# Optimization experiments

Measured on AMD Instinct MI355X. Metric: run time of the kernel, lower is better.

## Reference

```python
import jax, jax.numpy as jnp
import numpy as np

B, F, E = 2048, 200, 64

def setup_inputs() -> dict:
    key = jax.random.key(0)
    k1, k2 = jax.random.split(key)
    feature = jax.random.normal(k1, (B, F, E), dtype=jnp.float32)
    # nn.init.normal(weight, mean=0, std=0.01)
    weight = 0.01 * jax.random.normal(k2, (F, E, E), dtype=jnp.float32)
    return {"feature": feature, "weight": weight}

def reference(feature, weight):
    # biLinear[b,i,d] = sum_e feature[b,i,e] * weight[i,e,d]   (per-feature bilinear projection)
    bilinear = jnp.einsum('bie,ied->bid', feature, weight)
    # out[b,i,j] = sum_d bilinear[b,i,d] * feature[b,j,d]      (pairwise dot, avoids (B,F,F,E) temp)
    out = jnp.einsum('bid,bjd->bij', bilinear, feature)
    return out
```

## Files before the change

kernel.cpp:

```cpp
#include <hip/hip_runtime.h>

constexpr int Bb = 2048, Ff = 200, Ee = 64;

__global__ __launch_bounds__(256, 4)
void k1_bilinear(const float* __restrict__ feat, const float* __restrict__ wgt,
                 float* __restrict__ bil) {
    __shared__ float At[Ee * 64];
    __shared__ float Wl[Ee * 64];
    const int i  = blockIdx.y;
    const int b0 = blockIdx.x << 6;
    const int t  = threadIdx.x;

    {
        const float4* src = reinterpret_cast<const float4*>(wgt + (size_t)i * Ee * Ee);
        float4* dst = reinterpret_cast<float4*>(Wl);
        for (int q = t; q < 1024; q += 256) dst[q] = src[q];
    }
    for (int q = t; q < 1024; q += 256) {
        const int r  = q >> 4;
        const int e0 = (q & 15) << 2;
        const float4 v = *reinterpret_cast<const float4*>(
            feat + ((size_t)(b0 + r) * Ff + i) * Ee + e0);
        const int rf4 = r >> 2, rm = r & 3;
        const float vv[4] = {v.x, v.y, v.z, v.w};
#pragma unroll
        for (int k = 0; k < 4; ++k) {
            const int e = e0 + k;
            At[e * 64 + (((rf4 ^ ((e >> 2) & 7)) << 2) | rm)] = vv[k];
        }
    }
    __syncthreads();

    const int tx = t & 15, ty = t >> 4;
    const int d0 = tx << 2;
    float acc[4][4] = {};
#pragma unroll 4
    for (int e = 0; e < Ee; ++e) {
        const float4 a = *reinterpret_cast<const float4*>(
            At + e * 64 + ((ty ^ ((e >> 2) & 7)) << 2));
        const float4 w = *reinterpret_cast<const float4*>(Wl + e * 64 + d0);
        const float av[4] = {a.x, a.y, a.z, a.w};
        const float wv[4] = {w.x, w.y, w.z, w.w};
#pragma unroll
        for (int r = 0; r < 4; ++r)
#pragma unroll
            for (int c = 0; c < 4; ++c)
                acc[r][c] = fmaf(av[r], wv[c], acc[r][c]);
    }
#pragma unroll
    for (int r = 0; r < 4; ++r) {
        const float4 v = {acc[r][0], acc[r][1], acc[r][2], acc[r][3]};
        *reinterpret_cast<float4*>(
            bil + ((size_t)(b0 + (ty << 2) + r) * Ff + i) * Ee + d0) = v;
    }
}

__global__ __launch_bounds__(256, 2)
void k2_outer(const float* __restrict__ feat, const float* __restrict__ bil,
              float* __restrict__ out) {
    __shared__ float fT[Ee * 224];
    __shared__ float bT[Ee * 64];
    const int b = blockIdx.x;
    const int t = threadIdx.x;

    for (int q = t; q < 3200; q += 256) {
        const int j  = q >> 4;
        const int d0 = (q & 15) << 2;
        const float4 v = *reinterpret_cast<const float4*>(
            feat + ((size_t)b * Ff + j) * Ee + d0);
        const int jf4 = j >> 2, jm = j & 3;
        const float vv[4] = {v.x, v.y, v.z, v.w};
#pragma unroll
        for (int k = 0; k < 4; ++k) {
            const int d = d0 + k;
            fT[d * 224 + (((jf4 ^ ((d >> 2) & 7)) << 2) | jm)] = vv[k];
        }
    }

    const int jt = t % 50;
    const int it = t / 50;

    for (int i0 = 0; i0 < Ff; i0 += 40) {
        for (int q = t; q < 640; q += 256) {
            const int r  = q >> 4;
            const int d0 = (q & 15) << 2;
            const float4 v = *reinterpret_cast<const float4*>(
                bil + ((size_t)b * Ff + i0 + r) * Ee + d0);
            const int rf4 = r >> 2, rm = r & 3;
            const float vv[4] = {v.x, v.y, v.z, v.w};
#pragma unroll
            for (int k = 0; k < 4; ++k) {
                const int d = d0 + k;
                bT[d * 64 + (((rf4 ^ ((d >> 2) & 7)) << 2) | rm)] = vv[k];
            }
        }
        __syncthreads();

        if (t < 250) {
            float acc[8][4] = {};
#pragma unroll 4
            for (int d = 0; d < Ee; ++d) {
                const int c = (d >> 2) & 7;
                const float4 w4 = *reinterpret_cast<const float4*>(
                    fT + d * 224 + ((jt ^ c) << 2));
                const float4 a0 = *reinterpret_cast<const float4*>(
                    bT + d * 64 + (((it * 2) ^ c) << 2));
                const float4 a1 = *reinterpret_cast<const float4*>(
                    bT + d * 64 + (((it * 2 + 1) ^ c) << 2));
                const float av[8] = {a0.x, a0.y, a0.z, a0.w, a1.x, a1.y, a1.z, a1.w};
                const float wv[4] = {w4.x, w4.y, w4.z, w4.w};
#pragma unroll
                for (int r = 0; r < 8; ++r)
#pragma unroll
                    for (int c2 = 0; c2 < 4; ++c2)
                        acc[r][c2] = fmaf(av[r], wv[c2], acc[r][c2]);
            }
#pragma unroll
            for (int r = 0; r < 8; ++r) {
                const int i = i0 + it * 8 + r;
                const float4 v = {acc[r][0], acc[r][1], acc[r][2], acc[r][3]};
                *reinterpret_cast<float4*>(
                    out + ((size_t)b * Ff + i) * Ff + (jt << 2)) = v;
            }
        }
        __syncthreads();
    }
}

extern "C" void kernel_launch(void* const* d_in, const int* in_sizes, int n_in,
                              void* d_out, int out_size, void* d_ws, size_t ws_size,
                              hipStream_t stream) {
    const float* feat = (const float*)d_in[0];
    const float* wgt  = (const float*)d_in[1];
    float* out = (float*)d_out;
    float* bil = (float*)d_ws;

    k1_bilinear<<<dim3(Bb / 64, Ff), 256, 0, stream>>>(feat, wgt, bil);
    k2_outer<<<Bb, 256, 0, stream>>>(feat, bil, out);
}
```

Measured before the change: 558.8 us.

## Use split-bf16 MFMA for both bilinear and pairwise GEMMs

Both kernels are rewritten to run on bf16 MFMA instructions. Each fp32 operand is split into a high and a low bf16 half, and three MFMAs per tile approximate fp32 precision. The intermediate bilinear tensor is stored as packed hi/lo bf16 pairs. The second kernel now splits each batch across two blocks of 512 threads with per-wave 16-row strips. This trades scalar FMA work for matrix-core throughput, with roughly 3x the MFMA count and some loss of precision from dropping the lo*lo term. Output stores become scalar and strided per lane instead of float4.

```diff
diff --git a/kernel.cpp b/kernel.cpp
--- a/kernel.cpp
+++ b/kernel.cpp
@@ -1,129 +1,193 @@
 #include <hip/hip_runtime.h>
 
+
+typedef short bx8  __attribute__((ext_vector_type(8)));
+typedef float f32x4 __attribute__((ext_vector_type(4)));
+
 constexpr int Bb = 2048, Ff = 200, Ee = 64;
 
-__global__ __launch_bounds__(256, 4)
+__device__ __forceinline__ ushort bf16h(float x) {
+    uint u = __float_as_uint(x);
+    return (ushort)((u + 0x7FFFu + ((u >> 16) & 1u)) >> 16);
+}
+__device__ __forceinline__ float bf16f(ushort h) {
+    return __uint_as_float(((uint)h) << 16);
+}
+
+__global__ __launch_bounds__(256, 3)
 void k1_bilinear(const float* __restrict__ feat, const float* __restrict__ wgt,
-                 float* __restrict__ bil) {
-    __shared__ float At[Ee * 64];
-    __shared__ float Wl[Ee * 64];
+                 uint* __restrict__ bilP) {
+    __shared__ ushort fH[128 * 64], fL[128 * 64];
+    __shared__ ushort wH[64 * 64],  wL[64 * 64];
     const int i  = blockIdx.y;
-    const int b0 = blockIdx.x << 6;
+    const int b0 = blockIdx.x << 7;
     const int t  = threadIdx.x;
 
-    {
-        const float4* src = reinterpret_cast<const float4*>(wgt + (size_t)i * Ee * Ee);
-        float4* dst = reinterpret_cast<float4*>(Wl);
-        for (int q = t; q < 1024; q += 256) dst[q] = src[q];
-    }
-    for (int q = t; q < 1024; q += 256) {
-        const int r  = q >> 4;
-        const int e0 = (q & 15) << 2;
+    for (int q = t; q < 2048; q += 256) {
+        const int row = q >> 4, e0 = (q & 15) << 2;
         const float4 v = *reinterpret_cast<const float4*>(
-            feat + ((size_t)(b0 + r) * Ff + i) * Ee + e0);
-        const int rf4 = r >> 2, rm = r & 3;
+            feat + ((size_t)(b0 + row) * Ff + i) * Ee + e0);
         const float vv[4] = {v.x, v.y, v.z, v.w};
-#pragma unroll
-        for (int k = 0; k < 4; ++k) {
-            const int e = e0 + k;
-            At[e * 64 + (((rf4 ^ ((e >> 2) & 7)) << 2) | rm)] = vv[k];
-        }
+        ushort hh[4], ll[4];
+#pragma unroll
+        for (int j = 0; j < 4; ++j) {
+            hh[j] = bf16h(vv[j]);
+            ll[j] = bf16h(vv[j] - bf16f(hh[j]));
+        }
+        const int idx = row * 64 + (e0 ^ ((row & 7) << 3));
+        *reinterpret_cast<ushort4*>(&fH[idx]) = make_ushort4(hh[0], hh[1], hh[2], hh[3]);
+        *reinterpret_cast<ushort4*>(&fL[idx]) = make_ushort4(ll[0], ll[1], ll[2], ll[3]);
+    }
+    for (int q = t; q < 2048; q += 256) {
+        const int e = (q >> 6) << 1;
+        const int d = q & 63;
+        const float x0 = wgt[((size_t)i * Ee + e) * Ee + d];
+        const float x1 = wgt[((size_t)i * Ee + e + 1) * Ee + d];
+        const ushort h0 = bf16h(x0), h1 = bf16h(x1);
+        const ushort l0 = bf16h(x0 - bf16f(h0)), l1 = bf16h(x1 - bf16f(h1));
+        const int idx = d * 64 + (e ^ ((d & 7) << 3));
+        *reinterpret_cast<uint*>(&wH[idx]) = (uint)h0 | ((uint)h1 << 16);
+        *reinterpret_cast<uint*>(&wL[idx]) = (uint)l0 | ((uint)l1 << 16);
     }
     __syncthreads();
 
-    const int tx = t & 15, ty = t >> 4;
-    const int d0 = tx << 2;
-    float acc[4][4] = {};
-#pragma unroll 4
-    for (int e = 0; e < Ee; ++e) {
-        const float4 a = *reinterpret_cast<const float4*>(
-            At + e * 64 + ((ty ^ ((e >> 2) & 7)) << 2));
-        const float4 w = *reinterpret_cast<const float4*>(Wl + e * 64 + d0);
-        const float av[4] = {a.x, a.y, a.z, a.w};
-        const float wv[4] = {w.x, w.y, w.z, w.w};
-#pragma unroll
-        for (int r = 0; r < 4; ++r)
-#pragma unroll
-            for (int c = 0; c < 4; ++c)
-                acc[r][c] = fmaf(av[r], wv[c], acc[r][c]);
-    }
-#pragma unroll
-    for (int r = 0; r < 4; ++r) {
-        const float4 v = {acc[r][0], acc[r][1], acc[r][2], acc[r][3]};
-        *reinterpret_cast<float4*>(
-            bil + ((size_t)(b0 + (ty << 2) + r) * Ff + i) * Ee + d0) = v;
-    }
-}
-
-__global__ __launch_bounds__(256, 2)
-void k2_outer(const float* __restrict__ feat, const float* __restrict__ bil,
+    const int lane = t & 63, w = t >> 6;
+    const int r16 = lane & 15, g = lane >> 4;
+    f32x4 acc[2][4];
+#pragma unroll
+    for (int a = 0; a < 2; ++a)
+#pragma unroll
+        for (int j = 0; j < 4; ++j) acc[a][j] = (f32x4){0.f, 0.f, 0.f, 0.f};
+
+#pragma unroll
+    for (int ks = 0; ks < 2; ++ks) {
+        const int coff = ks * 32 + (g << 3);
+        bx8 AH[2], AL[2];
+#pragma unroll
+        for (int it = 0; it < 2; ++it) {
+            const int row = (w * 2 + it) * 16 + r16;
+            const int idx = row * 64 + (coff ^ ((row & 7) << 3));
+            AH[it] = *reinterpret_cast<const bx8*>(&fH[idx]);
+            AL[it] = *reinterpret_cast<const bx8*>(&fL[idx]);
+        }
+#pragma unroll
+        for (int jt = 0; jt < 4; ++jt) {
+            const int col = jt * 16 + r16;
+            const int idx = col * 64 + (coff ^ ((col & 7) << 3));
+            const bx8 BH = *reinterpret_cast<const bx8*>(&wH[idx]);
+            const bx8 BL = *reinterpret_cast<const bx8*>(&wL[idx]);
+#pragma unroll
+            for (int it = 0; it < 2; ++it) {
+                acc[it][jt] = __builtin_amdgcn_mfma_f32_16x16x32_bf16(AH[it], BH, acc[it][jt], 0, 0, 0);
+                acc[it][jt] = __builtin_amdgcn_mfma_f32_16x16x32_bf16(AH[it], BL, acc[it][jt], 0, 0, 0);
+                acc[it][jt] = __builtin_amdgcn_mfma_f32_16x16x32_bf16(AL[it], BH, acc[it][jt], 0, 0, 0);
+            }
+        }
+    }
+#pragma unroll
+    for (int it = 0; it < 2; ++it) {
+#pragma unroll
+        for (int jt = 0; jt < 4; ++jt) {
+            const int d = jt * 16 + r16;
+#pragma unroll
+            for (int reg = 0; reg < 4; ++reg) {
+                const int brow = b0 + (w * 2 + it) * 16 + (g << 2) + reg;
+                const float x = acc[it][jt][reg];
+                const ushort h = bf16h(x);
+                const ushort l = bf16h(x - bf16f(h));
+                bilP[((size_t)brow * Ff + i) * Ee + d] = (uint)h | ((uint)l << 16);
+            }
+        }
+    }
+}
+
+__global__ __launch_bounds__(512, 4)
+void k2_outer(const float* __restrict__ feat, const uint* __restrict__ bilP,
               float* __restrict__ out) {
-    __shared__ float fT[Ee * 224];
-    __shared__ float bT[Ee * 64];
-    const int b = blockIdx.x;
+    __shared__ ushort fjH[208 * 32], fjL[208 * 32];
+    __shared__ ushort aH[112 * 32],  aL[112 * 32];
+    const int ihalf = blockIdx.x, b = blockIdx.y;
     const int t = threadIdx.x;
-
-    for (int q = t; q < 3200; q += 256) {
-        const int j  = q >> 4;
-        const int d0 = (q & 15) << 2;
-        const float4 v = *reinterpret_cast<const float4*>(
-            feat + ((size_t)b * Ff + j) * Ee + d0);
-        const int jf4 = j >> 2, jm = j & 3;
-        const float vv[4] = {v.x, v.y, v.z, v.w};
-#pragma unroll
-        for (int k = 0; k < 4; ++k) {
-            const int d = d0 + k;
-            fT[d * 224 + (((jf4 ^ ((d >> 2) & 7)) << 2) | jm)] = vv[k];
-        }
-    }
-
-    const int jt = t % 50;
-    const int it = t / 50;
-
-    for (int i0 = 0; i0 < Ff; i0 += 40) {
-        for (int q = t; q < 640; q += 256) {
-            const int r  = q >> 4;
-            const int d0 = (q & 15) << 2;
-            const float4 v = *reinterpret_cast<const float4*>(
-                bil + ((size_t)b * Ff + i0 + r) * Ee + d0);
-            const int rf4 = r >> 2, rm = r & 3;
+    const int lane = t & 63, w = t >> 6;
+    const int r16 = lane & 15, g = lane >> 4;
+    const int nstrips = ihalf ? 6 : 7;
+    const int i0base = ihalf * 112;
+
+    f32x4 acc[13];
+#pragma unroll
+    for (int jt = 0; jt < 13; ++jt) acc[jt] = (f32x4){0.f, 0.f, 0.f, 0.f};
+
+#pragma unroll
+    for (int ks = 0; ks < 2; ++ks) {
+        for (int q = t; q < 1664; q += 512) {
+            const int j = q >> 3, c0 = (q & 7) << 2;
+            float4 v = {0.f, 0.f, 0.f, 0.f};
+            if (j < Ff)
+                v = *reinterpret_cast<const float4*>(
+                    feat + ((size_t)b * Ff + j) * Ee + ks * 32 + c0);
             const float vv[4] = {v.x, v.y, v.z, v.w};
-#pragma unroll
-            for (int k = 0; k < 4; ++k) {
-                const int d = d0 + k;
-                bT[d * 64 + (((rf4 ^ ((d >> 2) & 7)) << 2) | rm)] = vv[k];
-            }
+            ushort hh[4], ll[4];
+#pragma unroll
+            for (int u = 0; u < 4; ++u) {
+                hh[u] = bf16h(vv[u]);
+                ll[u] = bf16h(vv[u] - bf16f(hh[u]));
+            }
+            const int idx = j * 32 + (c0 ^ ((j & 3) << 3));
+            *reinterpret_cast<ushort4*>(&fjH[idx]) = make_ushort4(hh[0], hh[1], hh[2], hh[3]);
+            *reinterpret_cast<ushort4*>(&fjL[idx]) = make_ushort4(ll[0], ll[1], ll[2], ll[3]);
+        }
+        for (int q = t; q < 896; q += 512) {
+            const int r = q >> 3, c0 = (q & 7) << 2;
+            const int gi = i0base + r;
+            uint4 v = {0u, 0u, 0u, 0u};
+            if (gi < Ff)
+                v = *reinterpret_cast<const uint4*>(
+                    bilP + ((size_t)b * Ff + gi) * Ee + ks * 32 + c0);
+            const uint vv[4] = {v.x, v.y, v.z, v.w};
+            const int idx = r * 32 + (c0 ^ ((r & 3) << 3));
+            *reinterpret_cast<ushort4*>(&aH[idx]) = make_ushort4(
+                (ushort)(vv[0] & 0xFFFF), (ushort)(vv[1] & 0xFFFF),
+                (ushort)(vv[2] & 0xFFFF), (ushort)(vv[3] & 0xFFFF));
+            *reinterpret_cast<ushort4*>(&aL[idx]) = make_ushort4(
+                (ushort)(vv[0] >> 16), (ushort)(vv[1] >> 16),
+                (ushort)(vv[2] >> 16), (ushort)(vv[3] >> 16));
         }
         __syncthreads();
 
-        if (t < 250) {
-            float acc[8][4] = {};
-#pragma unroll 4
-            for (int d = 0; d < Ee; ++d) {
-                const int c = (d >> 2) & 7;
-                const float4 w4 = *reinterpret_cast<const float4*>(
-                    fT + d * 224 + ((jt ^ c) << 2));
-                const float4 a0 = *reinterpret_cast<const float4*>(
-                    bT + d * 64 + (((it * 2) ^ c) << 2));
-                const float4 a1 = *reinterpret_cast<const float4*>(
-                    bT + d * 64 + (((it * 2 + 1) ^ c) << 2));
-                const float av[8] = {a0.x, a0.y, a0.z, a0.w, a1.x, a1.y, a1.z, a1.w};
-                const float wv[4] = {w4.x, w4.y, w4.z, w4.w};
-#pragma unroll
-                for (int r = 0; r < 8; ++r)
-#pragma unroll
-                    for (int c2 = 0; c2 < 4; ++c2)
-                        acc[r][c2] = fmaf(av[r], wv[c2], acc[r][c2]);
-            }
-#pragma unroll
-            for (int r = 0; r < 8; ++r) {
-                const int i = i0 + it * 8 + r;
-                const float4 v = {acc[r][0], acc[r][1], acc[r][2], acc[r][3]};
-                *reinterpret_cast<float4*>(
-                    out + ((size_t)b * Ff + i) * Ff + (jt << 2)) = v;
+        if (w < nstrips) {
+            const int arow = w * 16 + r16;
+            const int cof = g << 3;
+            const int aidx = arow * 32 + (cof ^ ((arow & 3) << 3));
+            const bx8 AH = *reinterpret_cast<const bx8*>(&aH[aidx]);
+            const bx8 AL = *reinterpret_cast<const bx8*>(&aL[aidx]);
+#pragma unroll
+            for (int jt = 0; jt < 13; ++jt) {
+                const int jrow = jt * 16 + r16;
+                const int bidx = jrow * 32 + (cof ^ ((jrow & 3) << 3));
+                const bx8 BH = *reinterpret_cast<const bx8*>(&fjH[bidx]);
+                const bx8 BL = *reinterpret_cast<const bx8*>(&fjL[bidx]);
+                acc[jt] = __builtin_amdgcn_mfma_f32_16x16x32_bf16(AH, BH, acc[jt], 0, 0, 0);
+                acc[jt] = __builtin_amdgcn_mfma_f32_16x16x32_bf16(AH, BL, acc[jt], 0, 0, 0);
+                acc[jt] = __builtin_amdgcn_mfma_f32_16x16x32_bf16(AL, BH, acc[jt], 0, 0, 0);
             }
         }
         __syncthreads();
+    }
+
+    if (w < nstrips) {
+        const int ibase = i0base + w * 16 + (g << 2);
+#pragma unroll
+        for (int jt = 0; jt < 13; ++jt) {
+            const int col = jt * 16 + r16;
+            if (col < Ff) {
+#pragma unroll
+                for (int reg = 0; reg < 4; ++reg) {
+                    const int irow = ibase + reg;
+                    if (irow < Ff)
+                        out[((size_t)b * Ff + irow) * Ff + col] = acc[jt][reg];
+                }
+            }
+        }
     }
 }
 
@@ -133,8 +197,8 @@
     const float* feat = (const float*)d_in[0];
     const float* wgt  = (const float*)d_in[1];
     float* out = (float*)d_out;
-    float* bil = (float*)d_ws;
-
-    k1_bilinear<<<dim3(Bb / 64, Ff), 256, 0, stream>>>(feat, wgt, bil);
-    k2_outer<<<Bb, 256, 0, stream>>>(feat, bil, out);
-}
+    uint* bilP = (uint*)d_ws;
+
+    k1_bilinear<<<dim3(Bb / 128, Ff), 256, 0, stream>>>(feat, wgt, bilP);
+    k2_outer<<<dim3(2, Bb), 512, 0, stream>>>(feat, bilP, out);
+}
```

Result: faster. 535.0 us (-4.3%).
